# Performance work log

Hardware: AMD Instinct MI355X
Metric: run time of the kernel (lower is better)

## Reference

```python
import jax, jax.numpy as jnp
import numpy as np

B, S, MD, H = 8, 1024, 1024, 16
D = MD // H  # 64
# Faithful to torch: scale = (dim_per_head // num_heads) ** -0.5 (a quirk, not 1/sqrt(D))
SCALE = float((D // H) ** (-0.5))


def setup_inputs() -> dict:
    k0 = jax.random.key(0)
    ks = jax.random.split(k0, 11)
    w = 1.0 / np.sqrt(MD)
    mk = lambda k, shape, s: jax.random.normal(k, shape, dtype=jnp.float32) * s
    return {
        "query": mk(ks[0], (B, S, MD), 1.0),
        "key": mk(ks[1], (B, S, MD), 1.0),
        "value": mk(ks[2], (B, S, MD), 1.0),
        "Wq": mk(ks[3], (MD, MD), w), "bq": mk(ks[4], (MD,), w),
        "Wk": mk(ks[5], (MD, MD), w), "bk": mk(ks[6], (MD,), w),
        "Wv": mk(ks[7], (MD, MD), w), "bv": mk(ks[8], (MD,), w),
        "Wo": mk(ks[9], (MD, MD), w), "bo": mk(ks[10], (MD,), w),
    }


def reference(query, key, value, Wq, bq, Wk, bk, Wv, bv, Wo, bo):
    # Dropout is identity in eval mode (deterministic reference).
    Bq, T, _ = query.shape
    Sk = key.shape[1]
    q = query @ Wq + bq   # [B, T, H*D]
    k = key @ Wk + bk     # [B, S, H*D]
    v = value @ Wv + bv
    # Faithful replication of torch .view(B*H, -1, D): plain row-major reshape
    # (NOT a head transpose -- it chunks sequence/head indices together).
    q = q.reshape(Bq * H, T, D)
    k = k.reshape(Bq * H, Sk, D)
    v = v.reshape(Bq * H, Sk, D)
    attn = jnp.einsum('btd,bsd->bts', q, k) * SCALE          # [B*H, T, S]
    p = jax.nn.softmax(attn, axis=-1)
    ctx = jnp.einsum('bts,bsd->btd', p, v).reshape(Bq, T, H * D)
    output = ctx @ Wo + bo                                    # [B, T, MD]
    a = attn.reshape(Bq, H, T, Sk)
    attn_post = jax.nn.sigmoid(a).sum(axis=1) / H             # [B, T, S]
    return output, attn_post
```

## Files before the change

### kernel.cpp

```cpp
#include <hip/hip_runtime.h>


typedef __attribute__((ext_vector_type(8))) short bf16x8;
typedef __attribute__((ext_vector_type(4))) float f32x4;

static __device__ __forceinline__ short f2bf(float f) {
  union { float f; unsigned u; } v; v.f = f;
  unsigned lsb = (v.u >> 16) & 1u;
  v.u += 0x7fffu + lsb;
  return (short)(v.u >> 16);
}

static __device__ __forceinline__ short f2bf_rhu(float f) {
  union { float f; unsigned u; } v; v.f = f;
  v.u += 0x8000u;
  return (short)(v.u >> 16);
}

static __device__ __forceinline__ float exp2_hw(float x) {
  float r;
  asm("v_exp_f32 %0, %1" : "=v"(r) : "v"(x));
  return r;
}

#define L2E_HALF 0.72134752f

#define GLDS16(gp, lp) __builtin_amdgcn_global_load_lds( \
    (const __attribute__((address_space(1))) void*)(gp), \
    (__attribute__((address_space(3))) void*)(lp), 16, 0, 0)

struct Ptr4 { const float* s[4]; short* d[4]; };
struct Ptr3 { const float* s[3]; short* d[3]; };
struct QkvArgs { const short* A[3]; const short* B[3]; const float* bias[3]; short* C[3]; };

__global__ __launch_bounds__(256) void convt4(Ptr4 a)
{
  const float* __restrict__ src = a.s[blockIdx.z];
  short* __restrict__ dst = a.d[blockIdx.z];
  __shared__ float T[64][65];
  const int tid = threadIdx.x;
  const int c0 = blockIdx.x * 64, r0 = blockIdx.y * 64;
  {
    const int rr = tid >> 4, cc = (tid & 15) * 4;
    for (int i = 0; i < 4; ++i) {
      int row = rr + i * 16;
      const float4 v = *(const float4*)(src + (size_t)(r0 + row) * 1024 + c0 + cc);
      T[row][cc] = v.x; T[row][cc + 1] = v.y; T[row][cc + 2] = v.z; T[row][cc + 3] = v.w;
    }
  }
  __syncthreads();
  {
    const int rr = tid >> 3, cc = (tid & 7) * 8;
    for (int i = 0; i < 2; ++i) {
      int row = rr + i * 32;
      bf16x8 v;
      for (int j = 0; j < 8; ++j) v[j] = f2bf(T[cc + j][row]);
      *(bf16x8*)(dst + (size_t)(c0 + row) * 1024 + r0 + cc) = v;
    }
  }
}

__global__ __launch_bounds__(256) void cvt3(Ptr3 a)
{
  const float* __restrict__ src = a.s[blockIdx.z];
  short* __restrict__ dst = a.d[blockIdx.z];
  const size_t i = ((size_t)blockIdx.x * 256 + threadIdx.x) * 8;
  const float4 v0 = *(const float4*)(src + i);
  const float4 v1 = *(const float4*)(src + i + 4);
  bf16x8 o;
  o[0] = f2bf(v0.x); o[1] = f2bf(v0.y); o[2] = f2bf(v0.z); o[3] = f2bf(v0.w);
  o[4] = f2bf(v1.x); o[5] = f2bf(v1.y); o[6] = f2bf(v1.z); o[7] = f2bf(v1.w);
  *(bf16x8*)(dst + i) = o;
}

__global__ __launch_bounds__(256) void transp_v(
    const short* __restrict__ src, short* __restrict__ dst)
{
  __shared__ short T[64][72];
  const int g = blockIdx.y, t0 = blockIdx.x * 64;
  const short* s = src + (size_t)g * 65536 + (size_t)t0 * 64;
  short* d = dst + (size_t)g * 65536 + t0;
  const int r = threadIdx.x >> 3, c = (threadIdx.x & 7) * 8;
  for (int i = 0; i < 2; ++i) {
    bf16x8 v = *(const bf16x8*)(s + (size_t)(r + i * 32) * 64 + c);
    *(bf16x8*)(&T[r + i * 32][c]) = v;
  }
  __syncthreads();
  for (int i = 0; i < 2; ++i) {
    int dr = r + i * 32;
    bf16x8 v;
    for (int j = 0; j < 8; ++j) v[j] = T[c + j][dr];
    *(bf16x8*)(d + (size_t)dr * 1024 + c) = v;
  }
}

static __device__ __forceinline__ void gemm_body(
    const short* __restrict__ A, const short* __restrict__ BT,
    const float* __restrict__ bias, void* __restrict__ Cp, int mode)
{
  __shared__ short As[128 * 64];
  __shared__ short Bs[128 * 64];
  const int K = 1024, N = 1024;
  const int tid = threadIdx.x;
  const int lane = tid & 63, wave = tid >> 6;
  const int quad = lane >> 4, l16 = lane & 15;
  const int wm = (wave & 1) * 64, wn = (wave >> 1) * 64;
  const int bm = blockIdx.x * 128, bn = blockIdx.y * 128;

  f32x4 acc[4][4] = {};

  const int s_row = tid >> 3;
  const int s_col = (tid & 7) * 8;
  const int lds_base = wave * 512;

  for (int k0 = 0; k0 < K; k0 += 64) {
    for (int i = 0; i < 4; ++i) {
      int row = s_row + i * 32;
      GLDS16(A + (size_t)(bm + row) * K + k0 + s_col, &As[i * 2048 + lds_base]);
      GLDS16(BT + (size_t)(bn + row) * K + k0 + s_col, &Bs[i * 2048 + lds_base]);
    }
    __syncthreads();
    for (int ks = 0; ks < 2; ++ks) {
      bf16x8 af[4], bfr[4];
      for (int mi = 0; mi < 4; ++mi)
        af[mi] = *(const bf16x8*)(&As[(wm + mi * 16 + l16) * 64 + ks * 32 + quad * 8]);
      for (int ni = 0; ni < 4; ++ni)
        bfr[ni] = *(const bf16x8*)(&Bs[(wn + ni * 16 + l16) * 64 + ks * 32 + quad * 8]);
      for (int mi = 0; mi < 4; ++mi)
        for (int ni = 0; ni < 4; ++ni)
          acc[mi][ni] = __builtin_amdgcn_mfma_f32_16x16x32_bf16(af[mi], bfr[ni], acc[mi][ni], 0, 0, 0);
    }
    __syncthreads();
  }

  for (int ni = 0; ni < 4; ++ni) {
    int col = bn + wn + ni * 16 + l16;
    float bv = bias[col];
    for (int mi = 0; mi < 4; ++mi) {
      int row0 = bm + wm + mi * 16 + quad * 4;
      for (int r = 0; r < 4; ++r) {
        int row = row0 + r;
        float fv = acc[mi][ni][r] + bv;
        if (mode == 2) ((float*)Cp)[(size_t)row * N + col] = fv;
        else           ((short*)Cp)[(size_t)row * N + col] = f2bf(fv);
      }
    }
  }
}

__global__ __launch_bounds__(256) void gemm_bt16(
    const short* __restrict__ A, const short* __restrict__ BT,
    const float* __restrict__ bias, void* __restrict__ Cp, int mode)
{
  gemm_body(A, BT, bias, Cp, mode);
}

__global__ __launch_bounds__(256) void gemm_qkv(QkvArgs a)
{
  const int z = blockIdx.z;
  gemm_body(a.A[z], a.B[z], a.bias[z], a.C[z], 0);
}

__global__ __launch_bounds__(256) void attn_fused7(
    const short* __restrict__ Qp, const short* __restrict__ Kp,
    const short* __restrict__ VpT,
    short* __restrict__ ctx,
    float* __restrict__ attn_post)
{
  __shared__ short Plds[16][1032];
  __shared__ float red[16][4];

  const int tid = threadIdx.x;
  const int wave = tid >> 6, lane = tid & 63;
  const int quad = lane >> 4, l16 = lane & 15;
  const int orig = blockIdx.x;
  const int b = orig & 7;
  const int t0 = (orig >> 3) * 16;
  const int sbase = wave * 256;

  float sig[16][4] = {};

  for (int h = 0; h < 16; ++h) {
    const int g = b * 16 + h;
    const short* Qg = Qp + (size_t)g * 65536;
    const short* Kg = Kp + (size_t)g * 65536;
    const short* Vg = VpT + (size_t)g * 65536;

    bf16x8 aq0 = *(const bf16x8*)(Qg + (t0 + l16) * 64 + quad * 8);
    bf16x8 aq1 = *(const bf16x8*)(Qg + (t0 + l16) * 64 + 32 + quad * 8);

    float rsum[4] = {0.f, 0.f, 0.f, 0.f};

    bf16x8 kb0[4], kb1[4];
#pragma unroll
    for (int t = 0; t < 4; ++t) {
      int s = sbase + t * 16;
      kb0[t] = *(const bf16x8*)(Kg + (s + l16) * 64 + quad * 8);
      kb1[t] = *(const bf16x8*)(Kg + (s + l16) * 64 + 32 + quad * 8);
    }
#pragma unroll
    for (int tile = 0; tile < 16; ++tile) {
      const int slot = tile & 3;
      bf16x8 bk0 = kb0[slot], bk1 = kb1[slot];
      if (tile < 12) {
        int s = sbase + (tile + 4) * 16;
        kb0[slot] = *(const bf16x8*)(Kg + (s + l16) * 64 + quad * 8);
        kb1[slot] = *(const bf16x8*)(Kg + (s + l16) * 64 + 32 + quad * 8);
      }
      f32x4 c = {0.f, 0.f, 0.f, 0.f};
      c = __builtin_amdgcn_mfma_f32_16x16x32_bf16(aq0, bk0, c, 0, 0, 0);
      c = __builtin_amdgcn_mfma_f32_16x16x32_bf16(aq1, bk1, c, 0, 0, 0);
#pragma unroll
      for (int r = 0; r < 4; ++r) {
        float e = exp2_hw(c[r] * L2E_HALF);
        rsum[r] += e;
        Plds[quad * 4 + r][sbase + tile * 16 + l16] = f2bf_rhu(e);
        sig[tile][r] += e * __builtin_amdgcn_rcpf(1.f + e);
      }
    }
#pragma unroll
    for (int r = 0; r < 4; ++r)
      for (int mask = 1; mask < 16; mask <<= 1) rsum[r] += __shfl_xor(rsum[r], mask, 64);
    if (l16 == 0)
      for (int r = 0; r < 4; ++r) red[quad * 4 + r][wave] = rsum[r];
    __syncthreads();

    const short* Vw = Vg + (size_t)(wave * 16 + l16) * 1024;
    f32x4 a0 = {0.f,0.f,0.f,0.f}, a1 = a0, a2 = a0, a3 = a0;
#pragma unroll
    for (int sq = 0; sq < 8; ++sq) {
      bf16x8 p0 = *(const bf16x8*)(&Plds[l16][(sq * 4 + 0) * 32 + quad * 8]);
      bf16x8 p1 = *(const bf16x8*)(&Plds[l16][(sq * 4 + 1) * 32 + quad * 8]);
      bf16x8 p2 = *(const bf16x8*)(&Plds[l16][(sq * 4 + 2) * 32 + quad * 8]);
      bf16x8 p3 = *(const bf16x8*)(&Plds[l16][(sq * 4 + 3) * 32 + quad * 8]);
      bf16x8 v0 = *(const bf16x8*)(Vw + (sq * 4 + 0) * 32 + quad * 8);
      bf16x8 v1 = *(const bf16x8*)(Vw + (sq * 4 + 1) * 32 + quad * 8);
      bf16x8 v2 = *(const bf16x8*)(Vw + (sq * 4 + 2) * 32 + quad * 8);
      bf16x8 v3 = *(const bf16x8*)(Vw + (sq * 4 + 3) * 32 + quad * 8);
      a0 = __builtin_amdgcn_mfma_f32_16x16x32_bf16(p0, v0, a0, 0, 0, 0);
      a1 = __builtin_amdgcn_mfma_f32_16x16x32_bf16(p1, v1, a1, 0, 0, 0);
      a2 = __builtin_amdgcn_mfma_f32_16x16x32_bf16(p2, v2, a2, 0, 0, 0);
      a3 = __builtin_amdgcn_mfma_f32_16x16x32_bf16(p3, v3, a3, 0, 0, 0);
    }
    f32x4 cacc;
#pragma unroll
    for (int r = 0; r < 4; ++r) cacc[r] = (a0[r] + a1[r]) + (a2[r] + a3[r]);

    short* ctxg = ctx + (size_t)g * 65536 + t0 * 64;
#pragma unroll
    for (int r = 0; r < 4; ++r) {
      int row = quad * 4 + r;
      float s4 = red[row][0] + red[row][1] + red[row][2] + red[row][3];
      float inv = __builtin_amdgcn_rcpf(s4);
      ctxg[row * 64 + wave * 16 + l16] = f2bf(cacc[r] * inv);
    }
    __syncthreads();
  }

  float* ap_out = attn_post + (size_t)b * 1048576 + (size_t)t0 * 1024;
  for (int tile = 0; tile < 16; ++tile)
    for (int r = 0; r < 4; ++r)
      ap_out[(quad * 4 + r) * 1024 + sbase + tile * 16 + l16] = sig[tile][r] * 0.0625f;
}

extern "C" void kernel_launch(void* const* d_in, const int* in_sizes, int n_in,
                              void* d_out, int out_size, void* d_ws, size_t ws_size,
                              hipStream_t stream) {
  const float* query = (const float*)d_in[0];
  const float* key   = (const float*)d_in[1];
  const float* value = (const float*)d_in[2];
  const float* Wq = (const float*)d_in[3]; const float* bq = (const float*)d_in[4];
  const float* Wk = (const float*)d_in[5]; const float* bk = (const float*)d_in[6];
  const float* Wv = (const float*)d_in[7]; const float* bv = (const float*)d_in[8];
  const float* Wo = (const float*)d_in[9]; const float* bo = (const float*)d_in[10];

  float* out0 = (float*)d_out;
  float* attn_post = out0 + (8u << 20);

  short* WqT = (short*)d_ws;
  short* WkT = WqT + (1u << 20);
  short* WvT = WkT + (1u << 20);
  short* WoT = WvT + (1u << 20);
  short* Qp  = WoT + (1u << 20);
  short* Kp  = Qp + (8u << 20);
  short* VpT = Kp + (8u << 20);

  dim3 blk(256);
  const size_t NEED_BIG = (size_t)(60u << 20) * 2;

  convt4<<<dim3(16, 16, 4), blk, 0, stream>>>(
      Ptr4{{Wq, Wk, Wv, Wo}, {WqT, WkT, WvT, WoT}});

  short* ctx;
  if (ws_size >= NEED_BIG) {
    short* Xq = VpT + (8u << 20);
    short* Xk = Xq + (8u << 20);
    short* Xv = Xk + (8u << 20);
    short* Vflat = Xv + (8u << 20);
    ctx = Xq;

    cvt3<<<dim3(4096, 1, 3), blk, 0, stream>>>(Ptr3{{query, key, value}, {Xq, Xk, Xv}});
    gemm_qkv<<<dim3(64, 8, 3), blk, 0, stream>>>(
        QkvArgs{{Xq, Xk, Xv}, {WqT, WkT, WvT}, {bq, bk, bv}, {Qp, Kp, Vflat}});
    transp_v<<<dim3(16, 128), blk, 0, stream>>>(Vflat, VpT);
  } else {
    short* Xin = VpT + (8u << 20);
    short* Vflat = Xin + (8u << 20);
    ctx = Xin;

    cvt3<<<dim3(4096, 1, 1), blk, 0, stream>>>(Ptr3{{query, query, query}, {Xin, Xin, Xin}});
    gemm_bt16<<<dim3(64, 8), blk, 0, stream>>>(Xin, WqT, bq, Qp, 0);
    cvt3<<<dim3(4096, 1, 1), blk, 0, stream>>>(Ptr3{{key, key, key}, {Xin, Xin, Xin}});
    gemm_bt16<<<dim3(64, 8), blk, 0, stream>>>(Xin, WkT, bk, Kp, 0);
    cvt3<<<dim3(4096, 1, 1), blk, 0, stream>>>(Ptr3{{value, value, value}, {Xin, Xin, Xin}});
    gemm_bt16<<<dim3(64, 8), blk, 0, stream>>>(Xin, WvT, bv, Vflat, 0);
    transp_v<<<dim3(16, 128), blk, 0, stream>>>(Vflat, VpT);
  }

  attn_fused7<<<dim3(512), blk, 0, stream>>>(Qp, Kp, VpT, ctx, attn_post);
  gemm_bt16<<<dim3(64, 8), blk, 0, stream>>>(ctx, WoT, bo, out0, 2);
}
```

Before: 526.5 us.

## Process 32 query rows per attention block and swizzle GEMM block order

The fused attention kernel now handles two 16-row query tiles per block, so each K and V fragment loaded from global memory feeds two MFMA tiles. The grid is halved to 256 blocks and launch bounds are set to one block per CU. Separately, the GEMM remaps its linear block index so consecutive blocks share the same A rows across the 8 N-tiles, which should improve L2 reuse. In exchange the attention kernel keeps twice as many sigmoid accumulators (128 floats per thread), which raises register pressure, and 256 blocks may leave some CUs idle.

```diff
diff --git a/kernel.cpp b/kernel.cpp
--- a/kernel.cpp
+++ b/kernel.cpp
@@ -105,7 +105,10 @@
   const int lane = tid & 63, wave = tid >> 6;
   const int quad = lane >> 4, l16 = lane & 15;
   const int wm = (wave & 1) * 64, wn = (wave >> 1) * 64;
-  const int bm = blockIdx.x * 128, bn = blockIdx.y * 128;
+  const int lin = blockIdx.y * 64 + blockIdx.x;
+  const int bx = (lin >> 3) & 63;
+  const int by = lin & 7;
+  const int bm = bx * 128, bn = by * 128;
 
   f32x4 acc[4][4] = {};
 
@@ -161,24 +164,24 @@
   gemm_body(a.A[z], a.B[z], a.bias[z], a.C[z], 0);
 }
 
-__global__ __launch_bounds__(256) void attn_fused7(
+__global__ __launch_bounds__(256, 1) void attn_fused8(
     const short* __restrict__ Qp, const short* __restrict__ Kp,
     const short* __restrict__ VpT,
     short* __restrict__ ctx,
     float* __restrict__ attn_post)
 {
-  __shared__ short Plds[16][1032];
-  __shared__ float red[16][4];
+  __shared__ short Plds[32][1032];
+  __shared__ float red[32][4];
 
   const int tid = threadIdx.x;
   const int wave = tid >> 6, lane = tid & 63;
   const int quad = lane >> 4, l16 = lane & 15;
   const int orig = blockIdx.x;
   const int b = orig & 7;
-  const int t0 = (orig >> 3) * 16;
+  const int t0 = (orig >> 3) * 32;
   const int sbase = wave * 256;
 
-  float sig[16][4] = {};
+  float sig[2][16][4] = {};
 
   for (int h = 0; h < 16; ++h) {
     const int g = b * 16 + h;
@@ -186,10 +189,14 @@
     const short* Kg = Kp + (size_t)g * 65536;
     const short* Vg = VpT + (size_t)g * 65536;
 
-    bf16x8 aq0 = *(const bf16x8*)(Qg + (t0 + l16) * 64 + quad * 8);
-    bf16x8 aq1 = *(const bf16x8*)(Qg + (t0 + l16) * 64 + 32 + quad * 8);
-
-    float rsum[4] = {0.f, 0.f, 0.f, 0.f};
+    bf16x8 aq[2][2];
+#pragma unroll
+    for (int tt = 0; tt < 2; ++tt) {
+      aq[tt][0] = *(const bf16x8*)(Qg + (t0 + tt * 16 + l16) * 64 + quad * 8);
+      aq[tt][1] = *(const bf16x8*)(Qg + (t0 + tt * 16 + l16) * 64 + 32 + quad * 8);
+    }
+
+    float rsum[2][4] = {};
 
     bf16x8 kb0[4], kb1[4];
 #pragma unroll
@@ -207,60 +214,63 @@
         kb0[slot] = *(const bf16x8*)(Kg + (s + l16) * 64 + quad * 8);
         kb1[slot] = *(const bf16x8*)(Kg + (s + l16) * 64 + 32 + quad * 8);
       }
-      f32x4 c = {0.f, 0.f, 0.f, 0.f};
-      c = __builtin_amdgcn_mfma_f32_16x16x32_bf16(aq0, bk0, c, 0, 0, 0);
-      c = __builtin_amdgcn_mfma_f32_16x16x32_bf16(aq1, bk1, c, 0, 0, 0);
-#pragma unroll
+#pragma unroll
+      for (int tt = 0; tt < 2; ++tt) {
+        f32x4 c = {0.f, 0.f, 0.f, 0.f};
+        c = __builtin_amdgcn_mfma_f32_16x16x32_bf16(aq[tt][0], bk0, c, 0, 0, 0);
+        c = __builtin_amdgcn_mfma_f32_16x16x32_bf16(aq[tt][1], bk1, c, 0, 0, 0);
+#pragma unroll
+        for (int r = 0; r < 4; ++r) {
+          float e = exp2_hw(c[r] * L2E_HALF);
+          rsum[tt][r] += e;
+          Plds[tt * 16 + quad * 4 + r][sbase + tile * 16 + l16] = f2bf_rhu(e);
+          sig[tt][tile][r] += e * __builtin_amdgcn_rcpf(1.f + e);
+        }
+      }
+    }
+#pragma unroll
+    for (int tt = 0; tt < 2; ++tt)
+      for (int r = 0; r < 4; ++r)
+        for (int mask = 1; mask < 16; mask <<= 1)
+          rsum[tt][r] += __shfl_xor(rsum[tt][r], mask, 64);
+    if (l16 == 0)
+#pragma unroll
+      for (int tt = 0; tt < 2; ++tt)
+        for (int r = 0; r < 4; ++r)
+          red[tt * 16 + quad * 4 + r][wave] = rsum[tt][r];
+    __syncthreads();
+
+    const short* Vw = Vg + (size_t)(wave * 16 + l16) * 1024;
+    f32x4 acc[2][2] = {};
+#pragma unroll
+    for (int sl = 0; sl < 32; ++sl) {
+      bf16x8 v  = *(const bf16x8*)(Vw + sl * 32 + quad * 8);
+      bf16x8 p0 = *(const bf16x8*)(&Plds[l16][sl * 32 + quad * 8]);
+      bf16x8 p1 = *(const bf16x8*)(&Plds[16 + l16][sl * 32 + quad * 8]);
+      acc[0][sl & 1] = __builtin_amdgcn_mfma_f32_16x16x32_bf16(p0, v, acc[0][sl & 1], 0, 0, 0);
+      acc[1][sl & 1] = __builtin_amdgcn_mfma_f32_16x16x32_bf16(p1, v, acc[1][sl & 1], 0, 0, 0);
+    }
+
+    short* ctxg = ctx + (size_t)g * 65536 + t0 * 64;
+#pragma unroll
+    for (int tt = 0; tt < 2; ++tt)
       for (int r = 0; r < 4; ++r) {
-        float e = exp2_hw(c[r] * L2E_HALF);
-        rsum[r] += e;
-        Plds[quad * 4 + r][sbase + tile * 16 + l16] = f2bf_rhu(e);
-        sig[tile][r] += e * __builtin_amdgcn_rcpf(1.f + e);
+        int row = tt * 16 + quad * 4 + r;
+        float s4 = red[row][0] + red[row][1] + red[row][2] + red[row][3];
+        float inv = __builtin_amdgcn_rcpf(s4);
+        float cval = (acc[tt][0][r] + acc[tt][1][r]) * inv;
+        ctxg[row * 64 + wave * 16 + l16] = f2bf(cval);
       }
-    }
-#pragma unroll
-    for (int r = 0; r < 4; ++r)
-      for (int mask = 1; mask < 16; mask <<= 1) rsum[r] += __shfl_xor(rsum[r], mask, 64);
-    if (l16 == 0)
-      for (int r = 0; r < 4; ++r) red[quad * 4 + r][wave] = rsum[r];
     __syncthreads();
-
-    const short* Vw = Vg + (size_t)(wave * 16 + l16) * 1024;
-    f32x4 a0 = {0.f,0.f,0.f,0.f}, a1 = a0, a2 = a0, a3 = a0;
-#pragma unroll
-    for (int sq = 0; sq < 8; ++sq) {
-      bf16x8 p0 = *(const bf16x8*)(&Plds[l16][(sq * 4 + 0) * 32 + quad * 8]);
-      bf16x8 p1 = *(const bf16x8*)(&Plds[l16][(sq * 4 + 1) * 32 + quad * 8]);
-      bf16x8 p2 = *(const bf16x8*)(&Plds[l16][(sq * 4 + 2) * 32 + quad * 8]);
-      bf16x8 p3 = *(const bf16x8*)(&Plds[l16][(sq * 4 + 3) * 32 + quad * 8]);
-      bf16x8 v0 = *(const bf16x8*)(Vw + (sq * 4 + 0) * 32 + quad * 8);
-      bf16x8 v1 = *(const bf16x8*)(Vw + (sq * 4 + 1) * 32 + quad * 8);
-      bf16x8 v2 = *(const bf16x8*)(Vw + (sq * 4 + 2) * 32 + quad * 8);
-      bf16x8 v3 = *(const bf16x8*)(Vw + (sq * 4 + 3) * 32 + quad * 8);
-      a0 = __builtin_amdgcn_mfma_f32_16x16x32_bf16(p0, v0, a0, 0, 0, 0);
-      a1 = __builtin_amdgcn_mfma_f32_16x16x32_bf16(p1, v1, a1, 0, 0, 0);
-      a2 = __builtin_amdgcn_mfma_f32_16x16x32_bf16(p2, v2, a2, 0, 0, 0);
-      a3 = __builtin_amdgcn_mfma_f32_16x16x32_bf16(p3, v3, a3, 0, 0, 0);
-    }
-    f32x4 cacc;
-#pragma unroll
-    for (int r = 0; r < 4; ++r) cacc[r] = (a0[r] + a1[r]) + (a2[r] + a3[r]);
-
-    short* ctxg = ctx + (size_t)g * 65536 + t0 * 64;
-#pragma unroll
-    for (int r = 0; r < 4; ++r) {
-      int row = quad * 4 + r;
-      float s4 = red[row][0] + red[row][1] + red[row][2] + red[row][3];
-      float inv = __builtin_amdgcn_rcpf(s4);
-      ctxg[row * 64 + wave * 16 + l16] = f2bf(cacc[r] * inv);
-    }
-    __syncthreads();
   }
 
   float* ap_out = attn_post + (size_t)b * 1048576 + (size_t)t0 * 1024;
-  for (int tile = 0; tile < 16; ++tile)
-    for (int r = 0; r < 4; ++r)
-      ap_out[(quad * 4 + r) * 1024 + sbase + tile * 16 + l16] = sig[tile][r] * 0.0625f;
+#pragma unroll
+  for (int tt = 0; tt < 2; ++tt)
+    for (int tile = 0; tile < 16; ++tile)
+      for (int r = 0; r < 4; ++r)
+        ap_out[(tt * 16 + quad * 4 + r) * 1024 + sbase + tile * 16 + l16] =
+            sig[tt][tile][r] * 0.0625f;
 }
 
 extern "C" void kernel_launch(void* const* d_in, const int* in_sizes, int n_in,
@@ -317,6 +327,6 @@
     transp_v<<<dim3(16, 128), blk, 0, stream>>>(Vflat, VpT);
   }
 
-  attn_fused7<<<dim3(512), blk, 0, stream>>>(Qp, Kp, VpT, ctx, attn_post);
+  attn_fused8<<<dim3(256), blk, 0, stream>>>(Qp, Kp, VpT, ctx, attn_post);
   gemm_bt16<<<dim3(64, 8), blk, 0, stream>>>(ctx, WoT, bo, out0, 2);
 }
```

Result: faster. 445.7 us (-15.3%).
